# Performance work log

Hardware: AMD Instinct MI355X
Metric: run time of the kernel (lower is better)

## Reference

```python
import jax, jax.numpy as jnp
import numpy as np

N_NODES = 100000
N_FEAT = 256
N_EDGES = 3200000
N_CLUSTERS = 16
COLLAPSE_REG = 0.1


def setup_inputs() -> dict:
    key = jax.random.key(0)
    k1, k2, k3, k4 = jax.random.split(key, 4)
    features = jax.random.normal(k1, (N_NODES, N_FEAT), dtype=jnp.float32)
    edge_row = jax.random.randint(k2, (N_EDGES,), 0, N_NODES, dtype=jnp.int32)
    edge_col = jax.random.randint(k3, (N_EDGES,), 0, N_NODES, dtype=jnp.int32)
    edge_val = jnp.ones((N_EDGES,), dtype=jnp.float32)
    # orthogonal-ish init approximated by scaled normal (init does not affect math)
    W = jax.random.normal(k4, (N_FEAT, N_CLUSTERS), dtype=jnp.float32) / np.float32(np.sqrt(N_FEAT))
    b = jnp.zeros((N_CLUSTERS,), dtype=jnp.float32)
    return {"features": features, "W": W, "b": b,
            "edge_row": edge_row, "edge_col": edge_col, "edge_val": edge_val}


def reference(features, W, b, edge_row, edge_col, edge_val):
    n = features.shape[0]
    k = W.shape[1]
    # assignment softmax (dropout_rate=0 -> identity)
    assignments = jax.nn.softmax(features @ W + b, axis=1)  # [n, k]
    cluster_sizes = assignments.sum(axis=0)                  # [k]
    assignments_pooling = assignments / cluster_sizes        # [n, k]
    # degrees = sparse row sums of adjacency
    degrees = jax.ops.segment_sum(edge_val, edge_row, num_segments=n)[:, None]  # [n, 1]
    n_edges = degrees.sum() / 2
    # sparse mm: adjacency @ assignments via gather + segment_sum
    adj_assign = jax.ops.segment_sum(edge_val[:, None] * assignments[edge_col],
                                     edge_row, num_segments=n)  # [n, k]
    graph_pooled = assignments.T @ adj_assign                # [k, k]
    normalizer_left = assignments.T @ degrees                # [k, 1]
    normalizer_right = degrees.T @ assignments               # [1, k]
    normalizer = normalizer_left @ normalizer_right / (2 * n_edges)
    spectral_loss = -jnp.trace(graph_pooled - normalizer) / (2 * n_edges)
    collapse_loss = COLLAPSE_REG * (jnp.linalg.norm(cluster_sizes) / n
                                    * jnp.sqrt(jnp.float32(k)) - 1.0)
    features_pooled = jax.nn.selu(assignments_pooling.T @ features)  # [k, d]
    return features_pooled, assignments, spectral_loss, collapse_loss
```

## Files before the change

kernel.cpp:

```cpp
#include <hip/hip_runtime.h>
#include <math.h>

#define KC 16
#define DF 256

#define WS_POOLED 0
#define WS_CS     4096
#define WS_M      4112
#define WS_TR     4128
#define WS_ESUM   4129
#define WS_TOTAL  4130
#define SHDW_OFF_BYTES 16640


typedef float floatx2 __attribute__((ext_vector_type(2)));

__global__ void zero_ws_kernel(float* __restrict__ ws) {
  int i = blockIdx.x * blockDim.x + threadIdx.x;
  if (i < WS_TOTAL) ws[i] = 0.0f;
}

__device__ __forceinline__ void cvt16_fp8(uint4 u, float* f) {
  floatx2 p;
  p = __builtin_amdgcn_cvt_pk_f32_fp8(u.x, false); f[0] = p[0];  f[1] = p[1];
  p = __builtin_amdgcn_cvt_pk_f32_fp8(u.x, true);  f[2] = p[0];  f[3] = p[1];
  p = __builtin_amdgcn_cvt_pk_f32_fp8(u.y, false); f[4] = p[0];  f[5] = p[1];
  p = __builtin_amdgcn_cvt_pk_f32_fp8(u.y, true);  f[6] = p[0];  f[7] = p[1];
  p = __builtin_amdgcn_cvt_pk_f32_fp8(u.z, false); f[8] = p[0];  f[9] = p[1];
  p = __builtin_amdgcn_cvt_pk_f32_fp8(u.z, true);  f[10] = p[0]; f[11] = p[1];
  p = __builtin_amdgcn_cvt_pk_f32_fp8(u.w, false); f[12] = p[0]; f[13] = p[1];
  p = __builtin_amdgcn_cvt_pk_f32_fp8(u.w, true);  f[14] = p[0]; f[15] = p[1];
}

__device__ __forceinline__ void acc_edge1(uint4 A, uint4 B, float vq,
                                          float* m, float& tr, float& es) {
  float a[16], bb[16];
  cvt16_fp8(A, a); cvt16_fp8(B, bb);
  float d = 0.f;
  #pragma unroll
  for (int k = 0; k < 16; ++k) d += a[k] * bb[k];
  tr += vq * d; es += vq;
  #pragma unroll
  for (int k = 0; k < 16; ++k) m[k] += vq * a[k];
}

__global__ void __launch_bounds__(256, 2) assign_kernel(
    const float* __restrict__ F, const float* __restrict__ W,
    const float* __restrict__ b, float* __restrict__ S,
    unsigned* __restrict__ Sh, float* __restrict__ ws, int n) {
  __shared__ float Ft[2][32 * 257];
  __shared__ float cs_l[KC];
  const int t = threadIdx.x;
  if (t < KC) cs_l[t] = 0.0f;
  const int nb = blockIdx.x << 8;
  const int node = nb + t;
  const bool valid = node < n;
  const bool interior = (nb + 256 <= n);

  const int nl = t >> 3;
  const int jc = t & 7;

  float4 pref[8];
  auto load_chunk = [&](int s) {
    #pragma unroll
    for (int it = 0; it < 8; ++it) {
      const int nn = nl + (it << 5);
      if (interior || nb + nn < n)
        pref[it] = *(const float4*)&F[(size_t)(nb + nn) * DF + (s << 5) + (jc << 2)];
      else
        pref[it] = make_float4(0.f, 0.f, 0.f, 0.f);
    }
  };

  float acc[KC];
  #pragma unroll
  for (int k = 0; k < KC; ++k) acc[k] = 0.f;

  load_chunk(0);
  for (int s = 0; s < 8; ++s) {
    float* __restrict__ B = Ft[s & 1];
    #pragma unroll
    for (int it = 0; it < 8; ++it) {
      const int nn = nl + (it << 5);
      const int d0 = jc << 2;
      B[(d0 + 0) * 257 + nn] = pref[it].x;
      B[(d0 + 1) * 257 + nn] = pref[it].y;
      B[(d0 + 2) * 257 + nn] = pref[it].z;
      B[(d0 + 3) * 257 + nn] = pref[it].w;
    }
    __syncthreads();
    if (s < 7) load_chunk(s + 1);
    #pragma unroll
    for (int j = 0; j < 8; ++j) {
      const float fv0 = B[(4 * j + 0) * 257 + t];
      const float fv1 = B[(4 * j + 1) * 257 + t];
      const float fv2 = B[(4 * j + 2) * 257 + t];
      const float fv3 = B[(4 * j + 3) * 257 + t];
      const float* __restrict__ Wg = &W[(size_t)((s << 5) + (j << 2)) * KC];
      #pragma unroll
      for (int k = 0; k < KC; ++k)
        acc[k] += fv0 * Wg[k] + fv1 * Wg[KC + k]
                + fv2 * Wg[2 * KC + k] + fv3 * Wg[3 * KC + k];
    }
  }

  float mx = -1e30f;
  #pragma unroll
  for (int k = 0; k < KC; ++k) { acc[k] += b[k]; mx = fmaxf(mx, acc[k]); }
  float sum = 0.f;
  #pragma unroll
  for (int k = 0; k < KC; ++k) { acc[k] = __expf(acc[k] - mx); sum += acc[k]; }
  const float inv = 1.0f / sum;
  #pragma unroll
  for (int k = 0; k < KC; ++k) acc[k] *= inv;
  if (!valid) {
    #pragma unroll
    for (int k = 0; k < KC; ++k) acc[k] = 0.f;
  }
  if (valid) {
    float4* __restrict__ So = (float4*)&S[(size_t)node * KC];
    So[0] = make_float4(acc[0],  acc[1],  acc[2],  acc[3]);
    So[1] = make_float4(acc[4],  acc[5],  acc[6],  acc[7]);
    So[2] = make_float4(acc[8],  acc[9],  acc[10], acc[11]);
    So[3] = make_float4(acc[12], acc[13], acc[14], acc[15]);
    if (Sh) {
      unsigned w0, w1, w2, w3;
      w0 = __builtin_amdgcn_cvt_pk_fp8_f32(acc[0],  acc[1],  0,  false);
      w0 = __builtin_amdgcn_cvt_pk_fp8_f32(acc[2],  acc[3],  w0, true);
      w1 = __builtin_amdgcn_cvt_pk_fp8_f32(acc[4],  acc[5],  0,  false);
      w1 = __builtin_amdgcn_cvt_pk_fp8_f32(acc[6],  acc[7],  w1, true);
      w2 = __builtin_amdgcn_cvt_pk_fp8_f32(acc[8],  acc[9],  0,  false);
      w2 = __builtin_amdgcn_cvt_pk_fp8_f32(acc[10], acc[11], w2, true);
      w3 = __builtin_amdgcn_cvt_pk_fp8_f32(acc[12], acc[13], 0,  false);
      w3 = __builtin_amdgcn_cvt_pk_fp8_f32(acc[14], acc[15], w3, true);
      *(uint4*)&Sh[(size_t)node * 4] = make_uint4(w0, w1, w2, w3);
    }
  }
  #pragma unroll
  for (int off = 1; off < 64; off <<= 1) {
    #pragma unroll
    for (int k = 0; k < KC; ++k) acc[k] += __shfl_xor(acc[k], off);
  }
  if ((t & 63) == 0) {
    #pragma unroll
    for (int k = 0; k < KC; ++k) atomicAdd(&cs_l[k], acc[k]);
  }
  __syncthreads();
  if (t < KC) atomicAdd(&ws[WS_CS + t], cs_l[t]);
}

__global__ void __launch_bounds__(256) edge_kernel_fp8(
    const int* __restrict__ erow, const int* __restrict__ ecol,
    const float* __restrict__ evl, const uint4* __restrict__ S8,
    float* __restrict__ ws, int ne) {
  __shared__ float red[KC + 2];
  const int t = threadIdx.x;
  if (t < KC + 2) red[t] = 0.0f;
  __syncthreads();

  float m[KC];
  #pragma unroll
  for (int i = 0; i < KC; ++i) m[i] = 0.f;
  float tr = 0.f, es = 0.f;

  const int cbase = blockIdx.x << 11;
  const int base = cbase + t;
  int r[8], c[8];
  float v[8];
  if (cbase + 2048 <= ne) {
    #pragma unroll
    for (int i = 0; i < 8; ++i) {
      const int e = base + (i << 8);
      r[i] = erow[e]; c[i] = ecol[e]; v[i] = evl[e];
    }
  } else {
    #pragma unroll
    for (int i = 0; i < 8; ++i) {
      const int e = base + (i << 8);
      const bool ok = e < ne;
      r[i] = ok ? erow[e] : 0;
      c[i] = ok ? ecol[e] : 0;
      v[i] = ok ? evl[e] : 0.f;
    }
  }

  const uint4 A0 = S8[r[0]], B0 = S8[c[0]], A1 = S8[r[1]], B1 = S8[c[1]],
              A2 = S8[r[2]], B2 = S8[c[2]], A3 = S8[r[3]], B3 = S8[c[3]],
              A4 = S8[r[4]], B4 = S8[c[4]], A5 = S8[r[5]], B5 = S8[c[5]],
              A6 = S8[r[6]], B6 = S8[c[6]], A7 = S8[r[7]], B7 = S8[c[7]];
  acc_edge1(A0, B0, v[0], m, tr, es);
  acc_edge1(A1, B1, v[1], m, tr, es);
  acc_edge1(A2, B2, v[2], m, tr, es);
  acc_edge1(A3, B3, v[3], m, tr, es);
  acc_edge1(A4, B4, v[4], m, tr, es);
  acc_edge1(A5, B5, v[5], m, tr, es);
  acc_edge1(A6, B6, v[6], m, tr, es);
  acc_edge1(A7, B7, v[7], m, tr, es);

  #pragma unroll
  for (int off = 1; off < 64; off <<= 1) {
    tr += __shfl_xor(tr, off);
    es += __shfl_xor(es, off);
    #pragma unroll
    for (int i = 0; i < KC; ++i) m[i] += __shfl_xor(m[i], off);
  }
  if ((t & 63) == 0) {
    atomicAdd(&red[KC], tr);
    atomicAdd(&red[KC + 1], es);
    #pragma unroll
    for (int i = 0; i < KC; ++i) atomicAdd(&red[i], m[i]);
  }
  __syncthreads();
  if (t < KC)            atomicAdd(&ws[WS_M + t], red[t]);
  else if (t == KC)      atomicAdd(&ws[WS_TR], red[KC]);
  else if (t == KC + 1)  atomicAdd(&ws[WS_ESUM], red[KC + 1]);
}

__global__ void __launch_bounds__(256) edge_kernel_f32(
    const int* __restrict__ erow, const int* __restrict__ ecol,
    const float* __restrict__ evl, const float* __restrict__ S,
    float* __restrict__ ws, int ne) {
  __shared__ float red[KC + 2];
  const int t = threadIdx.x;
  if (t < KC + 2) red[t] = 0.0f;
  __syncthreads();
  float m[KC];
  #pragma unroll
  for (int i = 0; i < KC; ++i) m[i] = 0.f;
  float tr = 0.f, es = 0.f;
  const int stride = gridDim.x * blockDim.x;
  for (int e = blockIdx.x * blockDim.x + t; e < ne; e += stride) {
    const int r = erow[e];
    const int c = ecol[e];
    const float v = evl[e];
    const float4* __restrict__ Sr = (const float4*)(S + (size_t)r * KC);
    const float4* __restrict__ Sc = (const float4*)(S + (size_t)c * KC);
    const float4 a0 = Sr[0], a1 = Sr[1], a2 = Sr[2], a3 = Sr[3];
    const float4 b0 = Sc[0], b1 = Sc[1], b2 = Sc[2], b3 = Sc[3];
    float d = a0.x*b0.x + a0.y*b0.y + a0.z*b0.z + a0.w*b0.w
            + a1.x*b1.x + a1.y*b1.y + a1.z*b1.z + a1.w*b1.w
            + a2.x*b2.x + a2.y*b2.y + a2.z*b2.z + a2.w*b2.w
            + a3.x*b3.x + a3.y*b3.y + a3.z*b3.z + a3.w*b3.w;
    tr += v * d; es += v;
    m[0]+=v*a0.x; m[1]+=v*a0.y; m[2]+=v*a0.z; m[3]+=v*a0.w;
    m[4]+=v*a1.x; m[5]+=v*a1.y; m[6]+=v*a1.z; m[7]+=v*a1.w;
    m[8]+=v*a2.x; m[9]+=v*a2.y; m[10]+=v*a2.z; m[11]+=v*a2.w;
    m[12]+=v*a3.x; m[13]+=v*a3.y; m[14]+=v*a3.z; m[15]+=v*a3.w;
  }
  #pragma unroll
  for (int off = 1; off < 64; off <<= 1) {
    tr += __shfl_xor(tr, off);
    es += __shfl_xor(es, off);
    #pragma unroll
    for (int i = 0; i < KC; ++i) m[i] += __shfl_xor(m[i], off);
  }
  if ((t & 63) == 0) {
    atomicAdd(&red[KC], tr);
    atomicAdd(&red[KC + 1], es);
    #pragma unroll
    for (int i = 0; i < KC; ++i) atomicAdd(&red[i], m[i]);
  }
  __syncthreads();
  if (t < KC)            atomicAdd(&ws[WS_M + t], red[t]);
  else if (t == KC)      atomicAdd(&ws[WS_TR], red[KC]);
  else if (t == KC + 1)  atomicAdd(&ws[WS_ESUM], red[KC + 1]);
}

__global__ void __launch_bounds__(256) pool_kernel(
    const float* __restrict__ F, const float* __restrict__ S,
    float* __restrict__ ws, int n) {
  const int t = threadIdx.x;
  float acc[KC];
  #pragma unroll
  for (int i = 0; i < KC; ++i) acc[i] = 0.f;

  const int nch = n >> 5;
  for (int ch = blockIdx.x; ch < nch; ch += gridDim.x) {
    const int base = ch << 5;
    float fl[32];
    #pragma unroll
    for (int i = 0; i < 32; ++i)
      fl[i] = F[(size_t)(base + i) * DF + t];
    #pragma unroll
    for (int i = 0; i < 32; ++i) {
      const float4* __restrict__ Sr = (const float4*)(S + (size_t)(base + i) * KC);
      const float4 s0 = Sr[0], s1 = Sr[1], s2 = Sr[2], s3 = Sr[3];
      const float f = fl[i];
      acc[0]+=f*s0.x;  acc[1]+=f*s0.y;  acc[2]+=f*s0.z;  acc[3]+=f*s0.w;
      acc[4]+=f*s1.x;  acc[5]+=f*s1.y;  acc[6]+=f*s1.z;  acc[7]+=f*s1.w;
      acc[8]+=f*s2.x;  acc[9]+=f*s2.y;  acc[10]+=f*s2.z; acc[11]+=f*s2.w;
      acc[12]+=f*s3.x; acc[13]+=f*s3.y; acc[14]+=f*s3.z; acc[15]+=f*s3.w;
    }
  }
  if (blockIdx.x == 0) {
    for (int i2 = nch << 5; i2 < n; ++i2) {
      const float f = F[(size_t)i2 * DF + t];
      const float* __restrict__ Sr = S + (size_t)i2 * KC;
      #pragma unroll
      for (int kk = 0; kk < KC; ++kk) acc[kk] += f * Sr[kk];
    }
  }
  const int rot = blockIdx.x & 15;
  #pragma unroll
  for (int kk = 0; kk < KC; ++kk) {
    const int kidx = (kk + rot) & 15;
    atomicAdd(&ws[WS_POOLED + kidx * DF + t], acc[kidx]);
  }
}

__global__ void finalize_kernel(const float* __restrict__ ws,
                                float* __restrict__ out, int n) {
  const int idx = blockIdx.x * 256 + threadIdx.x;
  const float alpha = 1.6732632423543772f;
  const float scale = 1.0507009873554805f;
  if (idx < KC * DF) {
    const int k = idx >> 8;
    const float x = ws[WS_POOLED + idx] / ws[WS_CS + k];
    const float r = x > 0.f ? x : alpha * expm1f(x);
    out[idx] = scale * r;
  }
  if (idx == 0) {
    const float esum = ws[WS_ESUM];
    const float tr = ws[WS_TR];
    float sm2 = 0.f, sc2 = 0.f;
    for (int i = 0; i < KC; ++i) {
      const float mi = ws[WS_M + i];
      sm2 += mi * mi;
      const float ci = ws[WS_CS + i];
      sc2 += ci * ci;
    }
    const float spectral = -(tr - sm2 / esum) / esum;
    const float collapse = 0.1f * (sqrtf(sc2) / (float)n * 4.0f - 1.0f);
    const size_t off = (size_t)(KC * DF) + (size_t)n * KC;
    out[off] = spectral;
    out[off + 1] = collapse;
  }
}

extern "C" void kernel_launch(void* const* d_in, const int* in_sizes, int n_in,
                              void* d_out, int out_size, void* d_ws, size_t ws_size,
                              hipStream_t stream) {
  const float* F   = (const float*)d_in[0];
  const float* W   = (const float*)d_in[1];
  const float* b   = (const float*)d_in[2];
  const int* erow  = (const int*)d_in[3];
  const int* ecol  = (const int*)d_in[4];
  const float* evl = (const float*)d_in[5];
  const int n  = in_sizes[0] / DF;
  const int ne = in_sizes[3];
  float* out = (float*)d_out;
  float* S   = out + KC * DF;
  float* ws  = (float*)d_ws;

  const size_t shadow_bytes = (size_t)n * 16;
  const bool use_shadow = ws_size >= (size_t)SHDW_OFF_BYTES + shadow_bytes + 64;
  unsigned* Sh = use_shadow ? (unsigned*)((char*)d_ws + SHDW_OFF_BYTES) : nullptr;

  zero_ws_kernel<<<(WS_TOTAL + 255) / 256, 256, 0, stream>>>(ws);
  assign_kernel<<<(n + 255) / 256, 256, 0, stream>>>(F, W, b, S, Sh, ws, n);
  if (use_shadow) {
    const int eg = (ne + 2047) >> 11;
    edge_kernel_fp8<<<eg, 256, 0, stream>>>(erow, ecol, evl, (const uint4*)Sh, ws, ne);
  } else {
    edge_kernel_f32<<<2048, 256, 0, stream>>>(erow, ecol, evl, S, ws, ne);
  }
  pool_kernel<<<2048, 256, 0, stream>>>(F, S, ws, n);
  finalize_kernel<<<16, 256, 0, stream>>>(ws, out, n);
}
```

Before: 333.0 us.

## Fuse feature pooling into assignment kernel with 64-node tiles

Removes the separate pool kernel and computes the assignments-transposed-times-features partial sums inside the assignment kernel. Each block now handles 64 nodes. Four waves split the feature dimension for the projection, combine their partials through LDS, and then compute the softmax. The same feature tile is then reloaded, likely from cache, and multiplied by the block's assignments held in LDS. This avoids a second full pass over the feature matrix from DRAM and one kernel launch, at the cost of more blocks issuing global atomics on the pooled buffer and a longer kernel.

```diff
diff --git a/kernel.cpp b/kernel.cpp
--- a/kernel.cpp
+++ b/kernel.cpp
@@ -3,6 +3,7 @@
 
 #define KC 16
 #define DF 256
+#define ANB 64
 
 #define WS_POOLED 0
 #define WS_CS     4096
@@ -44,109 +45,159 @@
   for (int k = 0; k < 16; ++k) m[k] += vq * a[k];
 }
 
-__global__ void __launch_bounds__(256, 2) assign_kernel(
+__global__ void __launch_bounds__(256, 4) assign_fused_kernel(
     const float* __restrict__ F, const float* __restrict__ W,
     const float* __restrict__ b, float* __restrict__ S,
     unsigned* __restrict__ Sh, float* __restrict__ ws, int n) {
-  __shared__ float Ft[2][32 * 257];
-  __shared__ float cs_l[KC];
+  __shared__ float Ft[2][64 * 65];
+  __shared__ float Sl[64 * 20];
   const int t = threadIdx.x;
-  if (t < KC) cs_l[t] = 0.0f;
-  const int nb = blockIdx.x << 8;
-  const int node = nb + t;
-  const bool valid = node < n;
-  const bool interior = (nb + 256 <= n);
-
-  const int nl = t >> 3;
-  const int jc = t & 7;
-
-  float4 pref[8];
-  auto load_chunk = [&](int s) {
-    #pragma unroll
-    for (int it = 0; it < 8; ++it) {
-      const int nn = nl + (it << 5);
-      if (interior || nb + nn < n)
-        pref[it] = *(const float4*)&F[(size_t)(nb + nn) * DF + (s << 5) + (jc << 2)];
+  const int p  = t >> 6;
+  const int pu = __builtin_amdgcn_readfirstlane(p);
+  const int nl = t & 63;
+  const int base = blockIdx.x << 6;
+  const bool interior = (base + ANB <= n);
+
+  float4 pref[4];
+  auto load_chunk = [&](int c) {
+    #pragma unroll
+    for (int r = 0; r < 4; ++r) {
+      const int li = (r << 8) + t;
+      const int nd = li >> 4;
+      const int f4 = li & 15;
+      if (interior || base + nd < n)
+        pref[r] = *(const float4*)&F[(size_t)(base + nd) * DF + (c << 6) + (f4 << 2)];
       else
-        pref[it] = make_float4(0.f, 0.f, 0.f, 0.f);
+        pref[r] = make_float4(0.f, 0.f, 0.f, 0.f);
     }
   };
+  auto store_chunk = [&](int buf) {
+    float* __restrict__ Fb = Ft[buf];
+    #pragma unroll
+    for (int r = 0; r < 4; ++r) {
+      const int li = (r << 8) + t;
+      const int nd = li >> 4;
+      const int d0 = (li & 15) << 2;
+      Fb[(d0 + 0) * 65 + nd] = pref[r].x;
+      Fb[(d0 + 1) * 65 + nd] = pref[r].y;
+      Fb[(d0 + 2) * 65 + nd] = pref[r].z;
+      Fb[(d0 + 3) * 65 + nd] = pref[r].w;
+    }
+  };
 
   float acc[KC];
   #pragma unroll
   for (int k = 0; k < KC; ++k) acc[k] = 0.f;
 
   load_chunk(0);
-  for (int s = 0; s < 8; ++s) {
-    float* __restrict__ B = Ft[s & 1];
-    #pragma unroll
-    for (int it = 0; it < 8; ++it) {
-      const int nn = nl + (it << 5);
-      const int d0 = jc << 2;
-      B[(d0 + 0) * 257 + nn] = pref[it].x;
-      B[(d0 + 1) * 257 + nn] = pref[it].y;
-      B[(d0 + 2) * 257 + nn] = pref[it].z;
-      B[(d0 + 3) * 257 + nn] = pref[it].w;
-    }
+  #pragma unroll
+  for (int c = 0; c < 4; ++c) {
+    store_chunk(c & 1);
     __syncthreads();
-    if (s < 7) load_chunk(s + 1);
-    #pragma unroll
-    for (int j = 0; j < 8; ++j) {
-      const float fv0 = B[(4 * j + 0) * 257 + t];
-      const float fv1 = B[(4 * j + 1) * 257 + t];
-      const float fv2 = B[(4 * j + 2) * 257 + t];
-      const float fv3 = B[(4 * j + 3) * 257 + t];
-      const float* __restrict__ Wg = &W[(size_t)((s << 5) + (j << 2)) * KC];
+    if (c < 3) load_chunk(c + 1);
+    const float* __restrict__ Fb = Ft[c & 1];
+    #pragma unroll
+    for (int j = 0; j < 16; ++j) {
+      const float fv = Fb[((pu << 4) + j) * 65 + nl];
+      const float* __restrict__ Wg = &W[(size_t)((c << 6) + (pu << 4) + j) * KC];
       #pragma unroll
-      for (int k = 0; k < KC; ++k)
-        acc[k] += fv0 * Wg[k] + fv1 * Wg[KC + k]
-                + fv2 * Wg[2 * KC + k] + fv3 * Wg[3 * KC + k];
-    }
-  }
-
-  float mx = -1e30f;
-  #pragma unroll
-  for (int k = 0; k < KC; ++k) { acc[k] += b[k]; mx = fmaxf(mx, acc[k]); }
-  float sum = 0.f;
-  #pragma unroll
-  for (int k = 0; k < KC; ++k) { acc[k] = __expf(acc[k] - mx); sum += acc[k]; }
-  const float inv = 1.0f / sum;
-  #pragma unroll
-  for (int k = 0; k < KC; ++k) acc[k] *= inv;
-  if (!valid) {
-    #pragma unroll
-    for (int k = 0; k < KC; ++k) acc[k] = 0.f;
-  }
-  if (valid) {
-    float4* __restrict__ So = (float4*)&S[(size_t)node * KC];
-    So[0] = make_float4(acc[0],  acc[1],  acc[2],  acc[3]);
-    So[1] = make_float4(acc[4],  acc[5],  acc[6],  acc[7]);
-    So[2] = make_float4(acc[8],  acc[9],  acc[10], acc[11]);
-    So[3] = make_float4(acc[12], acc[13], acc[14], acc[15]);
-    if (Sh) {
-      unsigned w0, w1, w2, w3;
-      w0 = __builtin_amdgcn_cvt_pk_fp8_f32(acc[0],  acc[1],  0,  false);
-      w0 = __builtin_amdgcn_cvt_pk_fp8_f32(acc[2],  acc[3],  w0, true);
-      w1 = __builtin_amdgcn_cvt_pk_fp8_f32(acc[4],  acc[5],  0,  false);
-      w1 = __builtin_amdgcn_cvt_pk_fp8_f32(acc[6],  acc[7],  w1, true);
-      w2 = __builtin_amdgcn_cvt_pk_fp8_f32(acc[8],  acc[9],  0,  false);
-      w2 = __builtin_amdgcn_cvt_pk_fp8_f32(acc[10], acc[11], w2, true);
-      w3 = __builtin_amdgcn_cvt_pk_fp8_f32(acc[12], acc[13], 0,  false);
-      w3 = __builtin_amdgcn_cvt_pk_fp8_f32(acc[14], acc[15], w3, true);
-      *(uint4*)&Sh[(size_t)node * 4] = make_uint4(w0, w1, w2, w3);
-    }
-  }
-  #pragma unroll
-  for (int off = 1; off < 64; off <<= 1) {
-    #pragma unroll
-    for (int k = 0; k < KC; ++k) acc[k] += __shfl_xor(acc[k], off);
-  }
-  if ((t & 63) == 0) {
-    #pragma unroll
-    for (int k = 0; k < KC; ++k) atomicAdd(&cs_l[k], acc[k]);
-  }
-  __syncthreads();
-  if (t < KC) atomicAdd(&ws[WS_CS + t], cs_l[t]);
+      for (int k = 0; k < KC; ++k) acc[k] += fv * Wg[k];
+    }
+    __syncthreads();
+  }
+
+  float* __restrict__ red = &Ft[0][0];
+  #pragma unroll
+  for (int k4 = 0; k4 < 4; ++k4)
+    *(float4*)&red[(size_t)((p << 6) + nl) * KC + (k4 << 2)] =
+        make_float4(acc[k4 * 4 + 0], acc[k4 * 4 + 1],
+                    acc[k4 * 4 + 2], acc[k4 * 4 + 3]);
+  __syncthreads();
+
+  if (t < 64) {
+    float l[KC];
+    #pragma unroll
+    for (int k = 0; k < KC; ++k)
+      l[k] = red[t * KC + k] + red[(64 + t) * KC + k]
+           + red[(128 + t) * KC + k] + red[(192 + t) * KC + k] + b[k];
+    float mx = -1e30f;
+    #pragma unroll
+    for (int k = 0; k < KC; ++k) mx = fmaxf(mx, l[k]);
+    float sum = 0.f;
+    #pragma unroll
+    for (int k = 0; k < KC; ++k) { l[k] = __expf(l[k] - mx); sum += l[k]; }
+    const float inv = 1.0f / sum;
+    #pragma unroll
+    for (int k = 0; k < KC; ++k) l[k] *= inv;
+    const bool valid = base + t < n;
+    if (!valid) {
+      #pragma unroll
+      for (int k = 0; k < KC; ++k) l[k] = 0.f;
+    }
+    if (valid) {
+      const int node = base + t;
+      float4* __restrict__ So = (float4*)&S[(size_t)node * KC];
+      So[0] = make_float4(l[0],  l[1],  l[2],  l[3]);
+      So[1] = make_float4(l[4],  l[5],  l[6],  l[7]);
+      So[2] = make_float4(l[8],  l[9],  l[10], l[11]);
+      So[3] = make_float4(l[12], l[13], l[14], l[15]);
+      if (Sh) {
+        unsigned w0, w1, w2, w3;
+        w0 = __builtin_amdgcn_cvt_pk_fp8_f32(l[0],  l[1],  0,  false);
+        w0 = __builtin_amdgcn_cvt_pk_fp8_f32(l[2],  l[3],  w0, true);
+        w1 = __builtin_amdgcn_cvt_pk_fp8_f32(l[4],  l[5],  0,  false);
+        w1 = __builtin_amdgcn_cvt_pk_fp8_f32(l[6],  l[7],  w1, true);
+        w2 = __builtin_amdgcn_cvt_pk_fp8_f32(l[8],  l[9],  0,  false);
+        w2 = __builtin_amdgcn_cvt_pk_fp8_f32(l[10], l[11], w2, true);
+        w3 = __builtin_amdgcn_cvt_pk_fp8_f32(l[12], l[13], 0,  false);
+        w3 = __builtin_amdgcn_cvt_pk_fp8_f32(l[14], l[15], w3, true);
+        *(uint4*)&Sh[(size_t)node * 4] = make_uint4(w0, w1, w2, w3);
+      }
+    }
+    #pragma unroll
+    for (int k = 0; k < KC; ++k) Sl[t * 20 + k] = l[k];
+    #pragma unroll
+    for (int off = 1; off < 64; off <<= 1) {
+      #pragma unroll
+      for (int k = 0; k < KC; ++k) l[k] += __shfl_xor(l[k], off);
+    }
+    if (t == 0) {
+      #pragma unroll
+      for (int k = 0; k < KC; ++k) atomicAdd(&ws[WS_CS + k], l[k]);
+    }
+  }
+  __syncthreads();
+
+  float accp[16];
+  #pragma unroll
+  for (int i = 0; i < 16; ++i) accp[i] = 0.f;
+
+  load_chunk(0);
+  #pragma unroll
+  for (int c = 0; c < 4; ++c) {
+    store_chunk(c & 1);
+    __syncthreads();
+    if (c < 3) load_chunk(c + 1);
+    const float* __restrict__ Fb = Ft[c & 1];
+    const int kb = p << 2;
+    #pragma unroll 8
+    for (int node = 0; node < 64; ++node) {
+      const float fv = Fb[nl * 65 + node];
+      const float4 sv = *(const float4*)&Sl[node * 20 + kb];
+      accp[c * 4 + 0] += fv * sv.x;
+      accp[c * 4 + 1] += fv * sv.y;
+      accp[c * 4 + 2] += fv * sv.z;
+      accp[c * 4 + 3] += fv * sv.w;
+    }
+    __syncthreads();
+  }
+  #pragma unroll
+  for (int c = 0; c < 4; ++c) {
+    const int d = (c << 6) + nl;
+    #pragma unroll
+    for (int e = 0; e < 4; ++e)
+      atomicAdd(&ws[WS_POOLED + (size_t)((p << 2) + e) * DF + d], accp[c * 4 + e]);
+  }
 }
 
 __global__ void __launch_bounds__(256) edge_kernel_fp8(
@@ -266,48 +317,6 @@
   else if (t == KC + 1)  atomicAdd(&ws[WS_ESUM], red[KC + 1]);
 }
 
-__global__ void __launch_bounds__(256) pool_kernel(
-    const float* __restrict__ F, const float* __restrict__ S,
-    float* __restrict__ ws, int n) {
-  const int t = threadIdx.x;
-  float acc[KC];
-  #pragma unroll
-  for (int i = 0; i < KC; ++i) acc[i] = 0.f;
-
-  const int nch = n >> 5;
-  for (int ch = blockIdx.x; ch < nch; ch += gridDim.x) {
-    const int base = ch << 5;
-    float fl[32];
-    #pragma unroll
-    for (int i = 0; i < 32; ++i)
-      fl[i] = F[(size_t)(base + i) * DF + t];
-    #pragma unroll
-    for (int i = 0; i < 32; ++i) {
-      const float4* __restrict__ Sr = (const float4*)(S + (size_t)(base + i) * KC);
-      const float4 s0 = Sr[0], s1 = Sr[1], s2 = Sr[2], s3 = Sr[3];
-      const float f = fl[i];
-      acc[0]+=f*s0.x;  acc[1]+=f*s0.y;  acc[2]+=f*s0.z;  acc[3]+=f*s0.w;
-      acc[4]+=f*s1.x;  acc[5]+=f*s1.y;  acc[6]+=f*s1.z;  acc[7]+=f*s1.w;
-      acc[8]+=f*s2.x;  acc[9]+=f*s2.y;  acc[10]+=f*s2.z; acc[11]+=f*s2.w;
-      acc[12]+=f*s3.x; acc[13]+=f*s3.y; acc[14]+=f*s3.z; acc[15]+=f*s3.w;
-    }
-  }
-  if (blockIdx.x == 0) {
-    for (int i2 = nch << 5; i2 < n; ++i2) {
-      const float f = F[(size_t)i2 * DF + t];
-      const float* __restrict__ Sr = S + (size_t)i2 * KC;
-      #pragma unroll
-      for (int kk = 0; kk < KC; ++kk) acc[kk] += f * Sr[kk];
-    }
-  }
-  const int rot = blockIdx.x & 15;
-  #pragma unroll
-  for (int kk = 0; kk < KC; ++kk) {
-    const int kidx = (kk + rot) & 15;
-    atomicAdd(&ws[WS_POOLED + kidx * DF + t], acc[kidx]);
-  }
-}
-
 __global__ void finalize_kernel(const float* __restrict__ ws,
                                 float* __restrict__ out, int n) {
   const int idx = blockIdx.x * 256 + threadIdx.x;
@@ -357,13 +366,13 @@
   unsigned* Sh = use_shadow ? (unsigned*)((char*)d_ws + SHDW_OFF_BYTES) : nullptr;
 
   zero_ws_kernel<<<(WS_TOTAL + 255) / 256, 256, 0, stream>>>(ws);
-  assign_kernel<<<(n + 255) / 256, 256, 0, stream>>>(F, W, b, S, Sh, ws, n);
+  const int ag = (n + ANB - 1) >> 6;
+  assign_fused_kernel<<<ag, 256, 0, stream>>>(F, W, b, S, Sh, ws, n);
   if (use_shadow) {
     const int eg = (ne + 2047) >> 11;
     edge_kernel_fp8<<<eg, 256, 0, stream>>>(erow, ecol, evl, (const uint4*)Sh, ws, ne);
   } else {
     edge_kernel_f32<<<2048, 256, 0, stream>>>(erow, ecol, evl, S, ws, ne);
   }
-  pool_kernel<<<2048, 256, 0, stream>>>(F, S, ws, n);
   finalize_kernel<<<16, 256, 0, stream>>>(ws, out, n);
 }
```

New measurement: 577.6 us. 73.4% more time.

## Fuse edge and pooling kernels into one interleaved-role launch

Applied to the files above, without the earlier changes.

Merges the fp8 edge-gather kernel and the feature-pooling kernel into a single launch. Blocks alternate between pool and edge roles, so the bandwidth-bound feature streaming and the latency-bound random gathers run concurrently on the device. This removes one launch and the tail or drain gap between the two kernels. The cost is that the fused kernel keeps the register and LDS footprint of the heavier role, which may lower occupancy.

```diff
diff --git a/kernel.cpp b/kernel.cpp
--- a/kernel.cpp
+++ b/kernel.cpp
@@ -149,11 +149,10 @@
   if (t < KC) atomicAdd(&ws[WS_CS + t], cs_l[t]);
 }
 
-__global__ void __launch_bounds__(256) edge_kernel_fp8(
+__device__ __forceinline__ void edge_body_fp8(
     const int* __restrict__ erow, const int* __restrict__ ecol,
     const float* __restrict__ evl, const uint4* __restrict__ S8,
-    float* __restrict__ ws, int ne) {
-  __shared__ float red[KC + 2];
+    float* __restrict__ ws, int ne, int idx, float* __restrict__ red) {
   const int t = threadIdx.x;
   if (t < KC + 2) red[t] = 0.0f;
   __syncthreads();
@@ -163,7 +162,7 @@
   for (int i = 0; i < KC; ++i) m[i] = 0.f;
   float tr = 0.f, es = 0.f;
 
-  const int cbase = blockIdx.x << 11;
+  const int cbase = idx << 11;
   const int base = cbase + t;
   int r[8], c[8];
   float v[8];
@@ -214,6 +213,68 @@
   if (t < KC)            atomicAdd(&ws[WS_M + t], red[t]);
   else if (t == KC)      atomicAdd(&ws[WS_TR], red[KC]);
   else if (t == KC + 1)  atomicAdd(&ws[WS_ESUM], red[KC + 1]);
+}
+
+__device__ __forceinline__ void pool_body(
+    const float* __restrict__ F, const float* __restrict__ S,
+    float* __restrict__ ws, int n, int idx, int pg) {
+  const int t = threadIdx.x;
+  float acc[KC];
+  #pragma unroll
+  for (int i = 0; i < KC; ++i) acc[i] = 0.f;
+
+  const int nch = n >> 5;
+  for (int ch = idx; ch < nch; ch += pg) {
+    const int base = ch << 5;
+    float fl[32];
+    #pragma unroll
+    for (int i = 0; i < 32; ++i)
+      fl[i] = F[(size_t)(base + i) * DF + t];
+    #pragma unroll
+    for (int i = 0; i < 32; ++i) {
+      const float4* __restrict__ Sr = (const float4*)(S + (size_t)(base + i) * KC);
+      const float4 s0 = Sr[0], s1 = Sr[1], s2 = Sr[2], s3 = Sr[3];
+      const float f = fl[i];
+      acc[0]+=f*s0.x;  acc[1]+=f*s0.y;  acc[2]+=f*s0.z;  acc[3]+=f*s0.w;
+      acc[4]+=f*s1.x;  acc[5]+=f*s1.y;  acc[6]+=f*s1.z;  acc[7]+=f*s1.w;
+      acc[8]+=f*s2.x;  acc[9]+=f*s2.y;  acc[10]+=f*s2.z; acc[11]+=f*s2.w;
+      acc[12]+=f*s3.x; acc[13]+=f*s3.y; acc[14]+=f*s3.z; acc[15]+=f*s3.w;
+    }
+  }
+  if (idx == 0) {
+    for (int i2 = nch << 5; i2 < n; ++i2) {
+      const float f = F[(size_t)i2 * DF + t];
+      const float* __restrict__ Sr = S + (size_t)i2 * KC;
+      #pragma unroll
+      for (int kk = 0; kk < KC; ++kk) acc[kk] += f * Sr[kk];
+    }
+  }
+  const int rot = idx & 15;
+  #pragma unroll
+  for (int kk = 0; kk < KC; ++kk) {
+    const int kidx = (kk + rot) & 15;
+    atomicAdd(&ws[WS_POOLED + kidx * DF + t], acc[kidx]);
+  }
+}
+
+__global__ void __launch_bounds__(256) edge_pool_kernel(
+    const int* __restrict__ erow, const int* __restrict__ ecol,
+    const float* __restrict__ evl, const uint4* __restrict__ S8,
+    const float* __restrict__ F, const float* __restrict__ S,
+    float* __restrict__ ws, int ne, int n, int pg, int eg) {
+  __shared__ float red[KC + 2];
+  const int bid = blockIdx.x;
+  const int mn = pg < eg ? pg : eg;
+  const int nInter = 2 * mn;
+  int role, idx;
+  if (bid < nInter) { role = bid & 1; idx = bid >> 1; }
+  else {
+    const int rem = bid - nInter;
+    role = (pg > eg) ? 0 : 1;
+    idx = mn + rem;
+  }
+  if (role == 0) pool_body(F, S, ws, n, idx, pg);
+  else           edge_body_fp8(erow, ecol, evl, S8, ws, ne, idx, red);
 }
 
 __global__ void __launch_bounds__(256) edge_kernel_f32(
@@ -266,48 +327,6 @@
   else if (t == KC + 1)  atomicAdd(&ws[WS_ESUM], red[KC + 1]);
 }
 
-__global__ void __launch_bounds__(256) pool_kernel(
-    const float* __restrict__ F, const float* __restrict__ S,
-    float* __restrict__ ws, int n) {
-  const int t = threadIdx.x;
-  float acc[KC];
-  #pragma unroll
-  for (int i = 0; i < KC; ++i) acc[i] = 0.f;
-
-  const int nch = n >> 5;
-  for (int ch = blockIdx.x; ch < nch; ch += gridDim.x) {
-    const int base = ch << 5;
-    float fl[32];
-    #pragma unroll
-    for (int i = 0; i < 32; ++i)
-      fl[i] = F[(size_t)(base + i) * DF + t];
-    #pragma unroll
-    for (int i = 0; i < 32; ++i) {
-      const float4* __restrict__ Sr = (const float4*)(S + (size_t)(base + i) * KC);
-      const float4 s0 = Sr[0], s1 = Sr[1], s2 = Sr[2], s3 = Sr[3];
-      const float f = fl[i];
-      acc[0]+=f*s0.x;  acc[1]+=f*s0.y;  acc[2]+=f*s0.z;  acc[3]+=f*s0.w;
-      acc[4]+=f*s1.x;  acc[5]+=f*s1.y;  acc[6]+=f*s1.z;  acc[7]+=f*s1.w;
-      acc[8]+=f*s2.x;  acc[9]+=f*s2.y;  acc[10]+=f*s2.z; acc[11]+=f*s2.w;
-      acc[12]+=f*s3.x; acc[13]+=f*s3.y; acc[14]+=f*s3.z; acc[15]+=f*s3.w;
-    }
-  }
-  if (blockIdx.x == 0) {
-    for (int i2 = nch << 5; i2 < n; ++i2) {
-      const float f = F[(size_t)i2 * DF + t];
-      const float* __restrict__ Sr = S + (size_t)i2 * KC;
-      #pragma unroll
-      for (int kk = 0; kk < KC; ++kk) acc[kk] += f * Sr[kk];
-    }
-  }
-  const int rot = blockIdx.x & 15;
-  #pragma unroll
-  for (int kk = 0; kk < KC; ++kk) {
-    const int kidx = (kk + rot) & 15;
-    atomicAdd(&ws[WS_POOLED + kidx * DF + t], acc[kidx]);
-  }
-}
-
 __global__ void finalize_kernel(const float* __restrict__ ws,
                                 float* __restrict__ out, int n) {
   const int idx = blockIdx.x * 256 + threadIdx.x;
@@ -358,12 +377,16 @@
 
   zero_ws_kernel<<<(WS_TOTAL + 255) / 256, 256, 0, stream>>>(ws);
   assign_kernel<<<(n + 255) / 256, 256, 0, stream>>>(F, W, b, S, Sh, ws, n);
+
+  const int pg = 2048;
   if (use_shadow) {
     const int eg = (ne + 2047) >> 11;
-    edge_kernel_fp8<<<eg, 256, 0, stream>>>(erow, ecol, evl, (const uint4*)Sh, ws, ne);
+    edge_pool_kernel<<<pg + eg, 256, 0, stream>>>(
+        erow, ecol, evl, (const uint4*)Sh, F, S, ws, ne, n, pg, eg);
   } else {
     edge_kernel_f32<<<2048, 256, 0, stream>>>(erow, ecol, evl, S, ws, ne);
-  }
-  pool_kernel<<<2048, 256, 0, stream>>>(F, S, ws, n);
+    edge_pool_kernel<<<pg, 256, 0, stream>>>(
+        erow, ecol, evl, (const uint4*)nullptr, F, S, ws, ne, n, pg, 0);
+  }
   finalize_kernel<<<16, 256, 0, stream>>>(ws, out, n);
 }
```

New measurement: 290.4 us. -12.8%, faster.
